# Performance work log

Measured on AMD Instinct MI355X. Metric: run time of the kernel, lower is better.

## Reference

```python
import jax, jax.numpy as jnp
import numpy as np

EPS = 0.01                      # cfg.eps
INV_4PI = 1.0 / (4.0 * np.pi)   # 3D free-space Green's constant


def setup_inputs() -> dict:
    key = jax.random.key(0)
    k1, k2, k3 = jax.random.split(key, 3)
    B, M, d = 32768, 2048, 3
    return {
        "x_query": jax.random.normal(k1, (B, d), dtype=jnp.float32),
        "x_land": jax.random.normal(k2, (M, d), dtype=jnp.float32),
        "g_land": jax.random.normal(k3, (M,), dtype=jnp.float32),
    }


def reference(x_query, x_land, g_land):
    # Regularized 3D Poisson Green's function:
    #   G(x,y)      =  1/(4*pi) * (||x-y||^2 + eps^2)^(-1/2)
    #   grad_x G    = -1/(4*pi) * (x-y) * (||x-y||^2 + eps^2)^(-3/2)
    M = x_land.shape[0]
    r2 = (jnp.sum(x_query * x_query, axis=1)[:, None]
          - 2.0 * (x_query @ x_land.T)
          + jnp.sum(x_land * x_land, axis=1)[None, :])
    t = jnp.maximum(r2, 0.0) + EPS * EPS          # (B, M), regularized
    G = INV_4PI * jax.lax.rsqrt(t)                # (B, M)
    v_hat = (G * g_land[None, :]).sum(axis=1) / M # (B,)
    # fused gradient reduction: avoid materializing (B, M, d) dG.
    # sum_m g_m * dG = -1/(4pi) * [ x_q * sum_m c_m  -  c @ x_land ],
    # where c_m = g_m * t^(-3/2)
    c = g_land[None, :] * t ** (-1.5)             # (B, M)
    gradv_hat = -INV_4PI * (x_query * c.sum(axis=1, keepdims=True) - c @ x_land) / M
    return v_hat, gradv_hat
```

## Files before the change

kernel.cpp:

```cpp
#include <hip/hip_runtime.h>
#include <math.h>


#define EPS2    1e-4f
#define INV_4PI 0.07957747154594767f

constexpr int M_LAND = 2048;

typedef float f32x2 __attribute__((ext_vector_type(2)));

#define PAIR_COMPUTE(Q0_, Q1_, Q2_, QE_, AV_, AC_, AX_, AY_, AZ_) do { \
    f32x2 T; \
    asm("v_pk_add_f32 %0, %1, %2 op_sel:[0,1] op_sel_hi:[1,1]\n\t" \
        "v_pk_fma_f32 %0, %2, %3, %0 op_sel:[0,0,0] op_sel_hi:[0,1,1]\n\t" \
        "v_pk_fma_f32 %0, %4, %5, %0 op_sel:[1,0,0] op_sel_hi:[1,1,1]\n\t" \
        "v_pk_fma_f32 %0, %4, %6, %0 op_sel:[0,0,0] op_sel_hi:[0,1,1]" \
        : "=&v"(T) \
        : "v"(QE_), "v"(P2W), "v"(Q2_), "v"(P01), "v"(Q1_), "v"(Q0_)); \
    float ta = fmaxf(T.x, EPS2); \
    float tb = fmaxf(T.y, EPS2); \
    f32x2 S = { __builtin_amdgcn_rsqf(ta), __builtin_amdgcn_rsqf(tb) }; \
    f32x2 S2, S3; \
    asm("v_pk_mul_f32 %0, %7, %7 op_sel:[0,0] op_sel_hi:[1,1]\n\t" \
        "v_pk_mul_f32 %1, %0, %7 op_sel:[0,0] op_sel_hi:[1,1]\n\t" \
        "v_pk_fma_f32 %2, %8, %7, %2 op_sel:[1,0,0] op_sel_hi:[1,1,1]\n\t" \
        "v_pk_fma_f32 %3, %8, %1, %3 op_sel:[1,0,0] op_sel_hi:[1,1,1]\n\t" \
        "v_pk_fma_f32 %4, %1, %9, %4 op_sel:[0,0,0] op_sel_hi:[1,0,1]\n\t" \
        "v_pk_fma_f32 %5, %1, %9, %5 op_sel:[0,1,0] op_sel_hi:[1,1,1]\n\t" \
        "v_pk_fma_f32 %6, %1, %8, %6 op_sel:[0,0,0] op_sel_hi:[1,0,1]" \
        : "=&v"(S2), "=&v"(S3), \
          "+v"(AV_), "+v"(AC_), "+v"(AX_), "+v"(AY_), "+v"(AZ_) \
        : "v"(S), "v"(G2G), "v"(G01)); \
} while (0)

__global__ __launch_bounds__(512, 4)
void poisson_part_kernel(const float* __restrict__ xq,
                         const float* __restrict__ xl,
                         const float* __restrict__ gl,
                         float* __restrict__ ws)
{
    __shared__ float4 pack[512];
    __shared__ float4 gpack[512];
    __shared__ float  part[8][256][5];

    const int tid  = threadIdx.x;
    const int qblk = blockIdx.x >> 2;
    const int ms   = blockIdx.x & 3;

    {
        int jg = ms * 512 + tid;
        float l0 = xl[3*jg], l1 = xl[3*jg+1], l2 = xl[3*jg+2], g = gl[jg];
        float n2 = l0*l0 + l1*l1 + l2*l2 + EPS2;
        pack[tid]  = make_float4(-2.0f*l0, -2.0f*l1, -2.0f*l2, n2);
        gpack[tid] = make_float4(-2.0f*g*l0, -2.0f*g*l1, -2.0f*g*l2, g);
    }

    const int lane  = tid & 63;
    const int w     = tid >> 6;
    const int qbase = qblk * 256;

    const int qa = qbase + lane,       qbq = qbase + 64  + lane;
    const int qc = qbase + 128 + lane, qd  = qbase + 192 + lane;

    const float a0 = xq[3*qa], a1 = xq[3*qa+1], a2 = xq[3*qa+2];
    const float b0 = xq[3*qbq], b1 = xq[3*qbq+1], b2 = xq[3*qbq+2];
    const float c0 = xq[3*qc], c1 = xq[3*qc+1], c2 = xq[3*qc+2];
    const float d0 = xq[3*qd], d1 = xq[3*qd+1], d2 = xq[3*qd+2];

    f32x2 Q0a = {a0, b0}, Q1a = {a1, b1}, Q2a = {a2, b2};
    f32x2 QEa = {a0*a0 + a1*a1 + a2*a2, b0*b0 + b1*b1 + b2*b2};
    f32x2 Q0b = {c0, d0}, Q1b = {c1, d1}, Q2b = {c2, d2};
    f32x2 QEb = {c0*c0 + c1*c1 + c2*c2, d0*d0 + d1*d1 + d2*d2};

    f32x2 AVa = {0,0}, ACa = {0,0}, AXa = {0,0}, AYa = {0,0}, AZa = {0,0};
    f32x2 AVb = {0,0}, ACb = {0,0}, AXb = {0,0}, AYb = {0,0}, AZb = {0,0};

    __syncthreads();

    const int base = w * 64;
#pragma unroll 4
    for (int i = 0; i < 64; ++i) {
        const float4 p  = pack[base + i];
        const float4 gp = gpack[base + i];
        f32x2 P01 = {p.x,  p.y};
        f32x2 P2W = {p.z,  p.w};
        f32x2 G01 = {gp.x, gp.y};
        f32x2 G2G = {gp.z, gp.w};
        PAIR_COMPUTE(Q0a, Q1a, Q2a, QEa, AVa, ACa, AXa, AYa, AZa);
        PAIR_COMPUTE(Q0b, Q1b, Q2b, QEb, AVb, ACb, AXb, AYb, AZb);
    }

    part[w][lane][0] = AVa.x;  part[w][lane][1] = ACa.x;
    part[w][lane][2] = AXa.x;  part[w][lane][3] = AYa.x;  part[w][lane][4] = AZa.x;
    part[w][lane+64][0] = AVa.y;  part[w][lane+64][1] = ACa.y;
    part[w][lane+64][2] = AXa.y;  part[w][lane+64][3] = AYa.y;  part[w][lane+64][4] = AZa.y;
    part[w][lane+128][0] = AVb.x;  part[w][lane+128][1] = ACb.x;
    part[w][lane+128][2] = AXb.x;  part[w][lane+128][3] = AYb.x;  part[w][lane+128][4] = AZb.x;
    part[w][lane+192][0] = AVb.y;  part[w][lane+192][1] = ACb.y;
    part[w][lane+192][2] = AXb.y;  part[w][lane+192][3] = AYb.y;  part[w][lane+192][4] = AZb.y;

    __syncthreads();

    for (int s = tid; s < 1280; s += 512) {
        const int comp = s >> 8;
        const int qloc = s & 255;
        float acc = 0.f;
        #pragma unroll
        for (int ww = 0; ww < 8; ++ww) acc += part[ww][qloc][comp];
        ws[(size_t)blockIdx.x * 1280 + s] = acc;
    }
}

__global__ __launch_bounds__(512)
void poisson_combine_kernel(const float* __restrict__ ws,
                            const float* __restrict__ xq,
                            float* __restrict__ out, int B)
{
    const int gid  = blockIdx.x * 512 + threadIdx.x;
    const int q    = gid >> 2;
    const int cmp  = gid & 3;
    const int qblk = q >> 8;
    const int qloc = q & 255;
    const float* wbase = ws + (size_t)qblk * 4 * 1280;

    if (cmp == 0) {
        float s = 0.f;
        #pragma unroll
        for (int m = 0; m < 4; ++m) s += wbase[m*1280 + qloc];
        out[q] = s * (INV_4PI / (float)M_LAND);
    } else {
        float sc = 0.f, sy = 0.f;
        #pragma unroll
        for (int m = 0; m < 4; ++m) {
            sc += wbase[m*1280 + 256 + qloc];
            sy += wbase[m*1280 + (1+cmp)*256 + qloc];
        }
        const float qc = xq[3*q + (cmp-1)];
        out[B + 3*q + (cmp-1)] =
            (-INV_4PI / (float)M_LAND) * fmaf(qc, sc, 0.5f * sy);
    }
}

constexpr int NW_F  = 16;
constexpr int SL_F  = M_LAND / NW_F;
constexpr int QPB_F = 128;

__global__ __launch_bounds__(1024, 4)
void poisson_pk_kernel(const float* __restrict__ xq,
                       const float* __restrict__ xl,
                       const float* __restrict__ gl,
                       float* __restrict__ out, int B)
{
    __shared__ float4 pack[M_LAND];
    __shared__ float4 gpack[M_LAND];
    __shared__ float  part[NW_F][QPB_F][5];

    const int tid = threadIdx.x;
    for (int j = tid; j < M_LAND; j += 1024) {
        float l0 = xl[3*j], l1 = xl[3*j+1], l2 = xl[3*j+2], g = gl[j];
        float n2 = l0*l0 + l1*l1 + l2*l2 + EPS2;
        pack[j]  = make_float4(-2.0f*l0, -2.0f*l1, -2.0f*l2, n2);
        gpack[j] = make_float4(-2.0f*g*l0, -2.0f*g*l1, -2.0f*g*l2, g);
    }
    const int lane = tid & 63, w = tid >> 6;
    const int qbase = blockIdx.x * QPB_F;
    const int qa = qbase + lane, qb = qbase + 64 + lane;
    const float a0 = xq[3*qa], a1 = xq[3*qa+1], a2 = xq[3*qa+2];
    const float b0 = xq[3*qb], b1 = xq[3*qb+1], b2 = xq[3*qb+2];
    f32x2 Q0 = {a0, b0}, Q1 = {a1, b1}, Q2 = {a2, b2};
    f32x2 QE = {a0*a0 + a1*a1 + a2*a2, b0*b0 + b1*b1 + b2*b2};
    f32x2 AV = {0,0}, AC = {0,0}, AX = {0,0}, AY = {0,0}, AZ = {0,0};
    __syncthreads();

    const int base = w * SL_F;
#pragma unroll 8
    for (int i = 0; i < SL_F; ++i) {
        const float4 p  = pack[base + i];
        const float4 gp = gpack[base + i];
        f32x2 P01 = {p.x,  p.y};
        f32x2 P2W = {p.z,  p.w};
        f32x2 G01 = {gp.x, gp.y};
        f32x2 G2G = {gp.z, gp.w};
        PAIR_COMPUTE(Q0, Q1, Q2, QE, AV, AC, AX, AY, AZ);
    }
    part[w][lane][0] = AV.x;  part[w][lane][1] = AC.x;
    part[w][lane][2] = AX.x;  part[w][lane][3] = AY.x;  part[w][lane][4] = AZ.x;
    part[w][lane+64][0] = AV.y;  part[w][lane+64][1] = AC.y;
    part[w][lane+64][2] = AX.y;  part[w][lane+64][3] = AY.y;  part[w][lane+64][4] = AZ.y;
    __syncthreads();
    if (tid < 512) {
        const int q = tid >> 2, cmp = tid & 3, qg = qbase + q;
        if (cmp == 0) {
            float s = 0.f;
            #pragma unroll
            for (int ww = 0; ww < NW_F; ++ww) s += part[ww][q][0];
            out[qg] = s * (INV_4PI / (float)M_LAND);
        } else {
            float sc = 0.f, sy = 0.f;
            #pragma unroll
            for (int ww = 0; ww < NW_F; ++ww) {
                sc += part[ww][q][1];
                sy += part[ww][q][1 + cmp];
            }
            const float qc = xq[3*qg + (cmp-1)];
            out[B + 3*qg + (cmp-1)] =
                (-INV_4PI / (float)M_LAND) * fmaf(qc, sc, 0.5f * sy);
        }
    }
}

extern "C" void kernel_launch(void* const* d_in, const int* in_sizes, int n_in,
                              void* d_out, int out_size, void* d_ws, size_t ws_size,
                              hipStream_t stream)
{
    const float* xq = (const float*)d_in[0];
    const float* xl = (const float*)d_in[1];
    const float* gl = (const float*)d_in[2];
    float* out = (float*)d_out;

    const int B = in_sizes[0] / 3;

    const size_t need = (size_t)512 * 1280 * sizeof(float);
    if (ws_size >= need && B == 32768) {
        float* ws = (float*)d_ws;
        poisson_part_kernel<<<512, 512, 0, stream>>>(xq, xl, gl, ws);
        poisson_combine_kernel<<<256, 512, 0, stream>>>(ws, xq, out, B);
    } else {
        poisson_pk_kernel<<<B / QPB_F, 1024, 0, stream>>>(xq, xl, gl, out, B);
    }
}
```

Before: 28.09 us.

## Pre-pack landmarks and stream them via wave-uniform scalar loads

Adds a small pack kernel that writes per-landmark records (-2l, |l|^2+eps^2, g*l, g) to workspace once. The main kernel then reads these records from global memory with a wave-uniform address, so they can become scalar (SGPR) loads instead of LDS reads. Each thread handles one query with plain scalar FMAs instead of packed-pair inline asm. The cross-wave reduction and final combine now run inside the same kernel, which removes the separate combine kernel and the large workspace round trip. The trade-off is less per-thread ILP, since the packed two-query math is gone, and reliance on the compiler to actually emit scalar loads.

```diff
diff --git a/kernel.cpp b/kernel.cpp
--- a/kernel.cpp
+++ b/kernel.cpp
@@ -6,6 +6,96 @@
 #define INV_4PI 0.07957747154594767f
 
 constexpr int M_LAND = 2048;
+constexpr int NW     = 16;
+constexpr int SLICE  = M_LAND / NW;
+constexpr int QPB    = 64;
+
+__global__ void poisson_pack_kernel(const float* __restrict__ xl,
+                                    const float* __restrict__ gl,
+                                    float* __restrict__ ws)
+{
+    int j = blockIdx.x * 256 + threadIdx.x;
+    if (j < M_LAND) {
+        float l0 = xl[3*j], l1 = xl[3*j+1], l2 = xl[3*j+2], g = gl[j];
+        float* r = ws + 8*j;
+        r[0] = -2.0f*l0;  r[1] = -2.0f*l1;  r[2] = -2.0f*l2;
+        r[3] = l0*l0 + l1*l1 + l2*l2 + EPS2;
+        r[4] = g*l0;      r[5] = g*l1;      r[6] = g*l2;      r[7] = g;
+    }
+}
+
+__global__ __launch_bounds__(1024, 4)
+void poisson_sgpr_kernel(const float* __restrict__ xq,
+                         const float* __restrict__ rec,
+                         float* __restrict__ out, int B)
+{
+    __shared__ float part[NW][QPB][5];
+
+    const int tid   = threadIdx.x;
+    const int lane  = tid & 63;
+    const int w     = tid >> 6;
+    const int qbase = blockIdx.x * QPB;
+    const int q     = qbase + lane;
+
+    const float q0 = xq[3*q], q1 = xq[3*q+1], q2 = xq[3*q+2];
+    const float qe = q0*q0 + q1*q1 + q2*q2;
+
+    float av = 0.f, ac = 0.f, ax = 0.f, ay = 0.f, az = 0.f;
+
+    const int wu = __builtin_amdgcn_readfirstlane(w * SLICE);
+    const float* __restrict__ lm = rec + (size_t)wu * 8;
+
+#pragma unroll 4
+    for (int i = 0; i < SLICE; ++i) {
+        const float m0 = lm[8*i+0];
+        const float m1 = lm[8*i+1];
+        const float m2 = lm[8*i+2];
+        const float ne = lm[8*i+3];
+        const float h0 = lm[8*i+4];
+        const float h1 = lm[8*i+5];
+        const float h2 = lm[8*i+6];
+        const float g  = lm[8*i+7];
+
+        float t = fmaf(m0, q0, fmaf(m1, q1, fmaf(m2, q2, qe + ne)));
+        t = fmaxf(t, EPS2);
+        float s  = __builtin_amdgcn_rsqf(t);
+        float s2 = s * s;
+        float s3 = s2 * s;
+
+        av = fmaf(g,  s,  av);
+        ac = fmaf(g,  s3, ac);
+        ax = fmaf(s3, h0, ax);
+        ay = fmaf(s3, h1, ay);
+        az = fmaf(s3, h2, az);
+    }
+
+    part[w][lane][0] = av;  part[w][lane][1] = ac;
+    part[w][lane][2] = ax;  part[w][lane][3] = ay;  part[w][lane][4] = az;
+
+    __syncthreads();
+
+    if (tid < 256) {
+        const int ql  = tid >> 2;
+        const int cmp = tid & 3;
+        const int qg  = qbase + ql;
+        if (cmp == 0) {
+            float sum = 0.f;
+            #pragma unroll
+            for (int ww = 0; ww < NW; ++ww) sum += part[ww][ql][0];
+            out[qg] = sum * (INV_4PI / (float)M_LAND);
+        } else {
+            float sc = 0.f, sy = 0.f;
+            #pragma unroll
+            for (int ww = 0; ww < NW; ++ww) {
+                sc += part[ww][ql][1];
+                sy += part[ww][ql][1 + cmp];
+            }
+            const float qc = xq[3*qg + (cmp-1)];
+            out[B + 3*qg + (cmp-1)] =
+                (-INV_4PI / (float)M_LAND) * fmaf(qc, sc, -sy);
+        }
+    }
+}
 
 typedef float f32x2 __attribute__((ext_vector_type(2)));
 
@@ -33,114 +123,6 @@
         : "v"(S), "v"(G2G), "v"(G01)); \
 } while (0)
 
-__global__ __launch_bounds__(512, 4)
-void poisson_part_kernel(const float* __restrict__ xq,
-                         const float* __restrict__ xl,
-                         const float* __restrict__ gl,
-                         float* __restrict__ ws)
-{
-    __shared__ float4 pack[512];
-    __shared__ float4 gpack[512];
-    __shared__ float  part[8][256][5];
-
-    const int tid  = threadIdx.x;
-    const int qblk = blockIdx.x >> 2;
-    const int ms   = blockIdx.x & 3;
-
-    {
-        int jg = ms * 512 + tid;
-        float l0 = xl[3*jg], l1 = xl[3*jg+1], l2 = xl[3*jg+2], g = gl[jg];
-        float n2 = l0*l0 + l1*l1 + l2*l2 + EPS2;
-        pack[tid]  = make_float4(-2.0f*l0, -2.0f*l1, -2.0f*l2, n2);
-        gpack[tid] = make_float4(-2.0f*g*l0, -2.0f*g*l1, -2.0f*g*l2, g);
-    }
-
-    const int lane  = tid & 63;
-    const int w     = tid >> 6;
-    const int qbase = qblk * 256;
-
-    const int qa = qbase + lane,       qbq = qbase + 64  + lane;
-    const int qc = qbase + 128 + lane, qd  = qbase + 192 + lane;
-
-    const float a0 = xq[3*qa], a1 = xq[3*qa+1], a2 = xq[3*qa+2];
-    const float b0 = xq[3*qbq], b1 = xq[3*qbq+1], b2 = xq[3*qbq+2];
-    const float c0 = xq[3*qc], c1 = xq[3*qc+1], c2 = xq[3*qc+2];
-    const float d0 = xq[3*qd], d1 = xq[3*qd+1], d2 = xq[3*qd+2];
-
-    f32x2 Q0a = {a0, b0}, Q1a = {a1, b1}, Q2a = {a2, b2};
-    f32x2 QEa = {a0*a0 + a1*a1 + a2*a2, b0*b0 + b1*b1 + b2*b2};
-    f32x2 Q0b = {c0, d0}, Q1b = {c1, d1}, Q2b = {c2, d2};
-    f32x2 QEb = {c0*c0 + c1*c1 + c2*c2, d0*d0 + d1*d1 + d2*d2};
-
-    f32x2 AVa = {0,0}, ACa = {0,0}, AXa = {0,0}, AYa = {0,0}, AZa = {0,0};
-    f32x2 AVb = {0,0}, ACb = {0,0}, AXb = {0,0}, AYb = {0,0}, AZb = {0,0};
-
-    __syncthreads();
-
-    const int base = w * 64;
-#pragma unroll 4
-    for (int i = 0; i < 64; ++i) {
-        const float4 p  = pack[base + i];
-        const float4 gp = gpack[base + i];
-        f32x2 P01 = {p.x,  p.y};
-        f32x2 P2W = {p.z,  p.w};
-        f32x2 G01 = {gp.x, gp.y};
-        f32x2 G2G = {gp.z, gp.w};
-        PAIR_COMPUTE(Q0a, Q1a, Q2a, QEa, AVa, ACa, AXa, AYa, AZa);
-        PAIR_COMPUTE(Q0b, Q1b, Q2b, QEb, AVb, ACb, AXb, AYb, AZb);
-    }
-
-    part[w][lane][0] = AVa.x;  part[w][lane][1] = ACa.x;
-    part[w][lane][2] = AXa.x;  part[w][lane][3] = AYa.x;  part[w][lane][4] = AZa.x;
-    part[w][lane+64][0] = AVa.y;  part[w][lane+64][1] = ACa.y;
-    part[w][lane+64][2] = AXa.y;  part[w][lane+64][3] = AYa.y;  part[w][lane+64][4] = AZa.y;
-    part[w][lane+128][0] = AVb.x;  part[w][lane+128][1] = ACb.x;
-    part[w][lane+128][2] = AXb.x;  part[w][lane+128][3] = AYb.x;  part[w][lane+128][4] = AZb.x;
-    part[w][lane+192][0] = AVb.y;  part[w][lane+192][1] = ACb.y;
-    part[w][lane+192][2] = AXb.y;  part[w][lane+192][3] = AYb.y;  part[w][lane+192][4] = AZb.y;
-
-    __syncthreads();
-
-    for (int s = tid; s < 1280; s += 512) {
-        const int comp = s >> 8;
-        const int qloc = s & 255;
-        float acc = 0.f;
-        #pragma unroll
-        for (int ww = 0; ww < 8; ++ww) acc += part[ww][qloc][comp];
-        ws[(size_t)blockIdx.x * 1280 + s] = acc;
-    }
-}
-
-__global__ __launch_bounds__(512)
-void poisson_combine_kernel(const float* __restrict__ ws,
-                            const float* __restrict__ xq,
-                            float* __restrict__ out, int B)
-{
-    const int gid  = blockIdx.x * 512 + threadIdx.x;
-    const int q    = gid >> 2;
-    const int cmp  = gid & 3;
-    const int qblk = q >> 8;
-    const int qloc = q & 255;
-    const float* wbase = ws + (size_t)qblk * 4 * 1280;
-
-    if (cmp == 0) {
-        float s = 0.f;
-        #pragma unroll
-        for (int m = 0; m < 4; ++m) s += wbase[m*1280 + qloc];
-        out[q] = s * (INV_4PI / (float)M_LAND);
-    } else {
-        float sc = 0.f, sy = 0.f;
-        #pragma unroll
-        for (int m = 0; m < 4; ++m) {
-            sc += wbase[m*1280 + 256 + qloc];
-            sy += wbase[m*1280 + (1+cmp)*256 + qloc];
-        }
-        const float qc = xq[3*q + (cmp-1)];
-        out[B + 3*q + (cmp-1)] =
-            (-INV_4PI / (float)M_LAND) * fmaf(qc, sc, 0.5f * sy);
-    }
-}
-
 constexpr int NW_F  = 16;
 constexpr int SL_F  = M_LAND / NW_F;
 constexpr int QPB_F = 128;
@@ -220,11 +202,10 @@
 
     const int B = in_sizes[0] / 3;
 
-    const size_t need = (size_t)512 * 1280 * sizeof(float);
-    if (ws_size >= need && B == 32768) {
+    if (ws_size >= (size_t)(M_LAND * 8 * sizeof(float)) && (B % QPB) == 0) {
         float* ws = (float*)d_ws;
-        poisson_part_kernel<<<512, 512, 0, stream>>>(xq, xl, gl, ws);
-        poisson_combine_kernel<<<256, 512, 0, stream>>>(ws, xq, out, B);
+        poisson_pack_kernel<<<(M_LAND + 255) / 256, 256, 0, stream>>>(xl, gl, ws);
+        poisson_sgpr_kernel<<<B / QPB, 1024, 0, stream>>>(xq, ws, out, B);
     } else {
         poisson_pk_kernel<<<B / QPB_F, 1024, 0, stream>>>(xq, xl, gl, out, B);
     }
```

After: 33.31 us. +18.6%, slower.

## Halve per-thread queries and landmark splits, use 1024-thread blocks

Applied to the files above, without the earlier changes.

The part kernel is retiled. Each block now covers 128 queries against half of the landmarks, split across 16 waves, instead of 256 queries against a quarter. Each thread holds one packed query pair instead of two, and the combine step sums two partials instead of four. This doubles the resident waves per CU to hide latency better and cuts register pressure. In exchange there is less reuse of each shared-memory landmark load, less per-thread ILP, and a larger per-block cross-wave reduction.

```diff
diff --git a/kernel.cpp b/kernel.cpp
--- a/kernel.cpp
+++ b/kernel.cpp
@@ -33,22 +33,27 @@
         : "v"(S), "v"(G2G), "v"(G01)); \
 } while (0)
 
-__global__ __launch_bounds__(512, 4)
+constexpr int NW    = 16;
+constexpr int MHALF = M_LAND / 2;
+constexpr int SLICE = MHALF / NW;
+constexpr int QPB   = 128;
+
+__global__ __launch_bounds__(1024, 8)
 void poisson_part_kernel(const float* __restrict__ xq,
                          const float* __restrict__ xl,
                          const float* __restrict__ gl,
                          float* __restrict__ ws)
 {
-    __shared__ float4 pack[512];
-    __shared__ float4 gpack[512];
-    __shared__ float  part[8][256][5];
+    __shared__ float4 pack[MHALF];
+    __shared__ float4 gpack[MHALF];
+    __shared__ float  part[NW][QPB][5];
 
     const int tid  = threadIdx.x;
-    const int qblk = blockIdx.x >> 2;
-    const int ms   = blockIdx.x & 3;
+    const int qblk = blockIdx.x >> 1;
+    const int ms   = blockIdx.x & 1;
 
     {
-        int jg = ms * 512 + tid;
+        const int jg = ms * MHALF + tid;
         float l0 = xl[3*jg], l1 = xl[3*jg+1], l2 = xl[3*jg+2], g = gl[jg];
         float n2 = l0*l0 + l1*l1 + l2*l2 + EPS2;
         pack[tid]  = make_float4(-2.0f*l0, -2.0f*l1, -2.0f*l2, n2);
@@ -57,57 +62,44 @@
 
     const int lane  = tid & 63;
     const int w     = tid >> 6;
-    const int qbase = qblk * 256;
-
-    const int qa = qbase + lane,       qbq = qbase + 64  + lane;
-    const int qc = qbase + 128 + lane, qd  = qbase + 192 + lane;
+    const int qbase = qblk * QPB;
+    const int qa    = qbase + lane;
+    const int qb    = qbase + 64 + lane;
 
     const float a0 = xq[3*qa], a1 = xq[3*qa+1], a2 = xq[3*qa+2];
-    const float b0 = xq[3*qbq], b1 = xq[3*qbq+1], b2 = xq[3*qbq+2];
-    const float c0 = xq[3*qc], c1 = xq[3*qc+1], c2 = xq[3*qc+2];
-    const float d0 = xq[3*qd], d1 = xq[3*qd+1], d2 = xq[3*qd+2];
-
-    f32x2 Q0a = {a0, b0}, Q1a = {a1, b1}, Q2a = {a2, b2};
-    f32x2 QEa = {a0*a0 + a1*a1 + a2*a2, b0*b0 + b1*b1 + b2*b2};
-    f32x2 Q0b = {c0, d0}, Q1b = {c1, d1}, Q2b = {c2, d2};
-    f32x2 QEb = {c0*c0 + c1*c1 + c2*c2, d0*d0 + d1*d1 + d2*d2};
-
-    f32x2 AVa = {0,0}, ACa = {0,0}, AXa = {0,0}, AYa = {0,0}, AZa = {0,0};
-    f32x2 AVb = {0,0}, ACb = {0,0}, AXb = {0,0}, AYb = {0,0}, AZb = {0,0};
-
-    __syncthreads();
-
-    const int base = w * 64;
-#pragma unroll 4
-    for (int i = 0; i < 64; ++i) {
+    const float b0 = xq[3*qb], b1 = xq[3*qb+1], b2 = xq[3*qb+2];
+    f32x2 Q0 = {a0, b0}, Q1 = {a1, b1}, Q2 = {a2, b2};
+    f32x2 QE = {a0*a0 + a1*a1 + a2*a2, b0*b0 + b1*b1 + b2*b2};
+    f32x2 AV = {0,0}, AC = {0,0}, AX = {0,0}, AY = {0,0}, AZ = {0,0};
+
+    __syncthreads();
+
+    const int base = w * SLICE;
+#pragma unroll 2
+    for (int i = 0; i < SLICE; ++i) {
         const float4 p  = pack[base + i];
         const float4 gp = gpack[base + i];
         f32x2 P01 = {p.x,  p.y};
         f32x2 P2W = {p.z,  p.w};
         f32x2 G01 = {gp.x, gp.y};
         f32x2 G2G = {gp.z, gp.w};
-        PAIR_COMPUTE(Q0a, Q1a, Q2a, QEa, AVa, ACa, AXa, AYa, AZa);
-        PAIR_COMPUTE(Q0b, Q1b, Q2b, QEb, AVb, ACb, AXb, AYb, AZb);
-    }
-
-    part[w][lane][0] = AVa.x;  part[w][lane][1] = ACa.x;
-    part[w][lane][2] = AXa.x;  part[w][lane][3] = AYa.x;  part[w][lane][4] = AZa.x;
-    part[w][lane+64][0] = AVa.y;  part[w][lane+64][1] = ACa.y;
-    part[w][lane+64][2] = AXa.y;  part[w][lane+64][3] = AYa.y;  part[w][lane+64][4] = AZa.y;
-    part[w][lane+128][0] = AVb.x;  part[w][lane+128][1] = ACb.x;
-    part[w][lane+128][2] = AXb.x;  part[w][lane+128][3] = AYb.x;  part[w][lane+128][4] = AZb.x;
-    part[w][lane+192][0] = AVb.y;  part[w][lane+192][1] = ACb.y;
-    part[w][lane+192][2] = AXb.y;  part[w][lane+192][3] = AYb.y;  part[w][lane+192][4] = AZb.y;
-
-    __syncthreads();
-
-    for (int s = tid; s < 1280; s += 512) {
-        const int comp = s >> 8;
-        const int qloc = s & 255;
+        PAIR_COMPUTE(Q0, Q1, Q2, QE, AV, AC, AX, AY, AZ);
+    }
+
+    part[w][lane][0] = AV.x;  part[w][lane][1] = AC.x;
+    part[w][lane][2] = AX.x;  part[w][lane][3] = AY.x;  part[w][lane][4] = AZ.x;
+    part[w][lane+64][0] = AV.y;  part[w][lane+64][1] = AC.y;
+    part[w][lane+64][2] = AX.y;  part[w][lane+64][3] = AY.y;  part[w][lane+64][4] = AZ.y;
+
+    __syncthreads();
+
+    if (tid < 640) {
+        const int comp = tid >> 7;
+        const int qloc = tid & 127;
         float acc = 0.f;
         #pragma unroll
-        for (int ww = 0; ww < 8; ++ww) acc += part[ww][qloc][comp];
-        ws[(size_t)blockIdx.x * 1280 + s] = acc;
+        for (int ww = 0; ww < NW; ++ww) acc += part[ww][qloc][comp];
+        ws[(size_t)blockIdx.x * 640 + tid] = acc;
     }
 }
 
@@ -119,22 +111,16 @@
     const int gid  = blockIdx.x * 512 + threadIdx.x;
     const int q    = gid >> 2;
     const int cmp  = gid & 3;
-    const int qblk = q >> 8;
-    const int qloc = q & 255;
-    const float* wbase = ws + (size_t)qblk * 4 * 1280;
+    const int qblk = q >> 7;
+    const int qloc = q & 127;
+    const float* wbase = ws + (size_t)qblk * 2 * 640;
 
     if (cmp == 0) {
-        float s = 0.f;
-        #pragma unroll
-        for (int m = 0; m < 4; ++m) s += wbase[m*1280 + qloc];
+        float s = wbase[qloc] + wbase[640 + qloc];
         out[q] = s * (INV_4PI / (float)M_LAND);
     } else {
-        float sc = 0.f, sy = 0.f;
-        #pragma unroll
-        for (int m = 0; m < 4; ++m) {
-            sc += wbase[m*1280 + 256 + qloc];
-            sy += wbase[m*1280 + (1+cmp)*256 + qloc];
-        }
+        float sc = wbase[128 + qloc]            + wbase[640 + 128 + qloc];
+        float sy = wbase[(1+cmp)*128 + qloc]    + wbase[640 + (1+cmp)*128 + qloc];
         const float qc = xq[3*q + (cmp-1)];
         out[B + 3*q + (cmp-1)] =
             (-INV_4PI / (float)M_LAND) * fmaf(qc, sc, 0.5f * sy);
@@ -220,11 +206,11 @@
 
     const int B = in_sizes[0] / 3;
 
-    const size_t need = (size_t)512 * 1280 * sizeof(float);
-    if (ws_size >= need && B == 32768) {
+    const size_t need = (size_t)512 * 640 * sizeof(float);
+    if (ws_size >= need && (B % QPB) == 0) {
         float* ws = (float*)d_ws;
-        poisson_part_kernel<<<512, 512, 0, stream>>>(xq, xl, gl, ws);
-        poisson_combine_kernel<<<256, 512, 0, stream>>>(ws, xq, out, B);
+        poisson_part_kernel<<<(B / QPB) * 2, 1024, 0, stream>>>(xq, xl, gl, ws);
+        poisson_combine_kernel<<<(B * 4) / 512, 512, 0, stream>>>(ws, xq, out, B);
     } else {
         poisson_pk_kernel<<<B / QPB_F, 1024, 0, stream>>>(xq, xl, gl, out, B);
     }
```

Measured after the change: 28.09 us. No clear change (+0.0%).
